# Performance work log

Hardware: AMD Instinct MI355X
Metric: run time of the kernel (lower is better)

The kernel has to match this reference:

```python
import jax, jax.numpy as jnp
import numpy as np

K = 3          # kernel size (implied by 18/27 offset channels)
PAD = 1
STRIDE = 1


def setup_inputs() -> dict:
    key = jax.random.key(0)
    k0, k1, k2 = jax.random.split(key, 3)
    B, C, H, W = 4, 256, 64, 64
    Cout = 256
    x = jax.random.normal(k0, (B, C, H, W), jnp.float32)
    # offset/mask predicting conv: 18 offset + 9 mask channels (deform_group=1)
    w_off = jax.random.normal(k1, (27, C, K, K), jnp.float32) * 0.01
    b_off = jnp.zeros((27,), jnp.float32)
    # main deformable conv weight (bias=False)
    w = jax.random.normal(k2, (Cout, C, K, K), jnp.float32) * 0.05
    return {"x": x, "w_off": w_off, "b_off": b_off, "w": w}


def _modulated_dcn(x, w_off, b_off, w):
    B, C, H, W = x.shape
    KK = K * K
    # regular conv predicting offsets (+ mask)
    om = jax.lax.conv_general_dilated(
        x, w_off, (STRIDE, STRIDE), [(PAD, PAD), (PAD, PAD)],
        dimension_numbers=("NCHW", "OIHW", "NCHW")) + b_off[None, :, None, None]
    Ho, Wo = om.shape[2], om.shape[3]
    # channel layout: interleaved (dy, dx) per kernel tap, then 9 mask channels
    off = om[:, :2 * KK].reshape(B, KK, 2, Ho, Wo)
    mask = jax.nn.sigmoid(om[:, 2 * KK:3 * KK])            # (B, KK, Ho, Wo)

    ky, kx = jnp.meshgrid(jnp.arange(K), jnp.arange(K), indexing="ij")
    base_y = (jnp.arange(Ho) * STRIDE - PAD)[:, None]       # (Ho, 1)
    base_x = (jnp.arange(Wo) * STRIDE - PAD)[None, :]       # (1, Wo)
    # sampling positions p = p0 + pn + offset, shape (B, KK, Ho, Wo)
    py = base_y[None, None] + ky.reshape(KK)[None, :, None, None] + off[:, :, 0]
    px = base_x[None, None] + kx.reshape(KK)[None, :, None, None] + off[:, :, 1]

    y0f = jnp.floor(py)
    x0f = jnp.floor(px)
    ly = py - y0f
    lx = px - x0f
    y0 = y0f.astype(jnp.int32)
    x0 = x0f.astype(jnp.int32)

    xf = x.reshape(B, C, H * W)

    def samp(yi, xi):
        valid = ((yi >= 0) & (yi < H) & (xi >= 0) & (xi < W)).astype(x.dtype)
        idx = jnp.clip(yi, 0, H - 1) * W + jnp.clip(xi, 0, W - 1)
        v = jnp.take_along_axis(xf, idx.reshape(B, 1, -1), axis=2)
        return v.reshape(B, C, KK, Ho, Wo) * valid[:, None]

    # bilinear interpolation with zero padding outside the image
    v = (samp(y0,     x0    ) * ((1 - ly) * (1 - lx))[:, None]
         + samp(y0,     x0 + 1) * ((1 - ly) * lx)[:, None]
         + samp(y0 + 1, x0    ) * (ly * (1 - lx))[:, None]
         + samp(y0 + 1, x0 + 1) * (ly * lx)[:, None])
    v = v * mask[:, None]                                   # modulation
    # conv as contraction over (Cin, KK)
    return jnp.einsum("bckhw,ock->bohw", v, w.reshape(w.shape[0], C, KK))


def reference(x, w_off, b_off, w):
    return _modulated_dcn(x, w_off, b_off, w)
```

## Files before the change

### kernel.cpp

```cpp
#include <hip/hip_runtime.h>
#include <math.h>

#define HH 64
#define WW 64
#define CIN 256
#define COUT 256
#define KKT 9
#define HWSZ 4096
#define VP 260

typedef __bf16  v8bf   __attribute__((ext_vector_type(8)));
typedef float   v4f    __attribute__((ext_vector_type(4)));
typedef short   short8 __attribute__((ext_vector_type(8)));
typedef unsigned short ushort4v __attribute__((ext_vector_type(4)));

__device__ inline unsigned short f2bf(float f) {
    union { float f; unsigned u; } uf; uf.f = f;
    unsigned r = uf.u + 0x7fff + ((uf.u >> 16) & 1);
    return (unsigned short)(r >> 16);
}
__device__ inline float bf2f(unsigned short u) {
    union { unsigned u; float f; } uf; uf.u = ((unsigned)u) << 16;
    return uf.f;
}

__global__ __launch_bounds__(256) void k_prep(const float* __restrict__ x,
                                              const float* __restrict__ w,
                                              const float* __restrict__ w_off,
                                              unsigned short* __restrict__ x_t,
                                              unsigned short* __restrict__ wprep,
                                              unsigned short* __restrict__ woffp) {
    __shared__ float s_w[2304];
    int id  = blockIdx.x;
    int tid = threadIdx.x;
    if (id < 256) {
        int b  = id >> 6;
        int h  = id & 63;
        int px  = tid & 63;
        int oct = tid >> 6;
        const float* xr = x + (((size_t)b * CIN) * HH + h) * WW;
        unsigned short* orow = x_t + (((size_t)id) * WW + px) * CIN;
        for (int g = 0; g < 8; g++) {
            int cb = g * 32 + oct * 8;
            unsigned short v[8];
#pragma unroll
            for (int j = 0; j < 8; j++)
                v[j] = f2bf(xr[(size_t)(cb + j) * HWSZ + px]);
            *(short8*)(orow + cb) = *(short8*)v;
        }
    } else if (id < 512) {
        int o = id - 256;
        for (int i = tid; i < 2304; i += 256) s_w[i] = w[(size_t)o * 2304 + i];
        __syncthreads();
        for (int u = tid; u < 576; u += 256) {
            int t  = u >> 3;
            int kq = u & 7;
            unsigned short v[4];
#pragma unroll
            for (int j = 0; j < 4; j++) {
                int kp = t * 32 + kq * 4 + j;
                int kk = kp >> 8;
                int c  = kp & 255;
                v[j] = f2bf(s_w[c * 9 + kk]);
            }
            *(ushort4v*)&wprep[((size_t)(t * 256 + o)) * 32 + kq * 4] = *(ushort4v*)v;
        }
    } else {
        int t = id - 512;
#pragma unroll
        for (int i = 0; i < 4; i++) {
            int idx = i * 256 + tid;
            int och = idx >> 5;
            int ki  = idx & 31;
            int kp  = t * 32 + ki;
            int kk  = kp >> 8;
            int c   = kp & 255;
            float v = (och < 27) ? w_off[((size_t)och * 256 + c) * 9 + kk] : 0.f;
            woffp[(size_t)t * 1024 + idx] = f2bf(v);
        }
    }
}

__global__ __launch_bounds__(512, 4) void k_main(const unsigned short* __restrict__ x_t,
                                                 const unsigned short* __restrict__ wprep,
                                                 const unsigned short* __restrict__ woffp,
                                                 const float* __restrict__ b_off,
                                                 float* __restrict__ out) {
    int id    = blockIdx.x;
    int g     = id & 7;
    int phalf = (id >> 3) & 1;
    int hi    = (id >> 4) & 7;
    int b     = id >> 7;
    int h     = g * 8 + hi;
    int p0    = phalf * 32;
    int tid  = threadIdx.x;
    int lane = tid & 63;
    int oct  = tid >> 6;
    int m16  = lane & 15;
    int quad = lane >> 4;

    __shared__ union {
        unsigned short v[2][32 * VP];
        float red[4][32][33];
    } s_u;
    __shared__ int4   s_base[KKT][32];
    __shared__ float4 s_wt  [KKT][32];

    const unsigned short* xb = x_t + (size_t)b * HWSZ * CIN;

    {
        int ks  = oct >> 1;
        int ntw = oct & 1;
        v4f aco[2];
        aco[0] = (v4f)(0.f);
        aco[1] = (v4f)(0.f);
#pragma unroll 3
        for (int j = 0; j < 18; j++) {
            int t  = j * 4 + ks;
            int kk = t >> 3;
            int ch = t & 7;
            int ky = kk / 3 - 1;
            int kx = kk - 3 * (kk / 3) - 1;
            const unsigned short* wp = woffp + (size_t)t * 1024;
            short8 af0 = *(const short8*)(wp + m16 * 32 + quad * 8);
            short8 af1 = *(const short8*)(wp + (16 + m16) * 32 + quad * 8);
            int y  = h + ky;
            int xg = p0 + ntw * 16 + m16 + kx;
            short8 bfr = (short8)0;
            if ((unsigned)y < HH && (unsigned)xg < WW)
                bfr = *(const short8*)(xb + ((size_t)y * WW + xg) * CIN + ch * 32 + quad * 8);
            aco[0] = __builtin_amdgcn_mfma_f32_16x16x32_bf16(
                __builtin_bit_cast(v8bf, af0), __builtin_bit_cast(v8bf, bfr), aco[0], 0, 0, 0);
            aco[1] = __builtin_amdgcn_mfma_f32_16x16x32_bf16(
                __builtin_bit_cast(v8bf, af1), __builtin_bit_cast(v8bf, bfr), aco[1], 0, 0, 0);
        }
#pragma unroll
        for (int mt = 0; mt < 2; mt++)
#pragma unroll
            for (int r = 0; r < 4; r++)
                s_u.red[ks][mt * 16 + quad * 4 + r][ntw * 16 + m16] = aco[mt][r];
    }
    __syncthreads();

    for (int i = tid; i < KKT * 32; i += 512) {
        int kk = i >> 5;
        int pl = i & 31;
        int p  = p0 + pl;
        float offy = s_u.red[0][2 * kk][pl]     + s_u.red[1][2 * kk][pl]
                   + s_u.red[2][2 * kk][pl]     + s_u.red[3][2 * kk][pl]     + b_off[2 * kk];
        float offx = s_u.red[0][2 * kk + 1][pl] + s_u.red[1][2 * kk + 1][pl]
                   + s_u.red[2][2 * kk + 1][pl] + s_u.red[3][2 * kk + 1][pl] + b_off[2 * kk + 1];
        float mv   = s_u.red[0][18 + kk][pl]    + s_u.red[1][18 + kk][pl]
                   + s_u.red[2][18 + kk][pl]    + s_u.red[3][18 + kk][pl]    + b_off[18 + kk];
        int ky = kk / 3, kx = kk - 3 * (kk / 3);
        float py = (float)(h - 1 + ky) + offy;
        float px = (float)(p - 1 + kx) + offx;
        float y0f = floorf(py);
        float x0f = floorf(px);
        float ly = py - y0f, lx = px - x0f;
        int y0 = (int)y0f, x0 = (int)x0f;
        float m = 1.f / (1.f + __expf(-mv));
        bool yv0 = (unsigned)y0       < HH;
        bool yv1 = (unsigned)(y0 + 1) < HH;
        bool xv0 = (unsigned)x0       < WW;
        bool xv1 = (unsigned)(x0 + 1) < WW;
        int y0c = min(max(y0, 0), HH - 1);
        int y1c = min(max(y0 + 1, 0), HH - 1);
        int x0c = min(max(x0, 0), WW - 1);
        int x1c = min(max(x0 + 1, 0), WW - 1);
        s_base[kk][pl] = make_int4((y0c * WW + x0c) * CIN, (y0c * WW + x1c) * CIN,
                                   (y1c * WW + x0c) * CIN, (y1c * WW + x1c) * CIN);
        s_wt[kk][pl] = make_float4(
            (yv0 && xv0) ? (1.f - ly) * (1.f - lx) * m : 0.f,
            (yv0 && xv1) ? (1.f - ly) * lx         * m : 0.f,
            (yv1 && xv0) ? ly * (1.f - lx)         * m : 0.f,
            (yv1 && xv1) ? ly * lx                 * m : 0.f);
    }
    __syncthreads();

    v4f acc[2][2];
#pragma unroll
    for (int mt = 0; mt < 2; mt++)
#pragma unroll
        for (int nt = 0; nt < 2; nt++) acc[mt][nt] = (v4f)(0.f);

    const unsigned short* xc = xb + lane * 4;

    for (int kk = 0; kk < KKT; kk++) {
        unsigned short* vbuf = s_u.v[kk & 1];

#pragma unroll
        for (int i = 0; i < 4; i++) {
            int pl = oct * 4 + i;
            int4   bp = s_base[kk][pl];
            float4 wt = s_wt[kk][pl];
            ushort4v t0 = *(const ushort4v*)(xc + bp.x);
            ushort4v t1 = *(const ushort4v*)(xc + bp.y);
            ushort4v t2 = *(const ushort4v*)(xc + bp.z);
            ushort4v t3 = *(const ushort4v*)(xc + bp.w);
            unsigned short vv[4];
#pragma unroll
            for (int j = 0; j < 4; j++) {
                float val = wt.x * bf2f(t0[j]) + wt.y * bf2f(t1[j])
                          + wt.z * bf2f(t2[j]) + wt.w * bf2f(t3[j]);
                vv[j] = f2bf(val);
            }
            *(ushort4v*)&vbuf[pl * VP + lane * 4] = *(ushort4v*)vv;
        }
        __syncthreads();

#pragma unroll
        for (int ch = 0; ch < 8; ch++) {
            int t = kk * 8 + ch;
            const unsigned short* wp = wprep + ((size_t)t * 256 + oct * 32) * 32;
            short8 af0 = *(const short8*)(wp + m16 * 32 + quad * 8);
            short8 af1 = *(const short8*)(wp + (16 + m16) * 32 + quad * 8);
            short8 bfr[2];
#pragma unroll
            for (int nt = 0; nt < 2; nt++)
                bfr[nt] = *(const short8*)&vbuf[(nt * 16 + m16) * VP + ch * 32 + quad * 8];
#pragma unroll
            for (int nt = 0; nt < 2; nt++) {
                acc[0][nt] = __builtin_amdgcn_mfma_f32_16x16x32_bf16(
                    __builtin_bit_cast(v8bf, af0), __builtin_bit_cast(v8bf, bfr[nt]),
                    acc[0][nt], 0, 0, 0);
                acc[1][nt] = __builtin_amdgcn_mfma_f32_16x16x32_bf16(
                    __builtin_bit_cast(v8bf, af1), __builtin_bit_cast(v8bf, bfr[nt]),
                    acc[1][nt], 0, 0, 0);
            }
        }
    }

    float* ob = out + ((size_t)b * COUT) * HWSZ + h * WW + p0;
#pragma unroll
    for (int mt = 0; mt < 2; mt++)
#pragma unroll
        for (int nt = 0; nt < 2; nt++)
#pragma unroll
            for (int r = 0; r < 4; r++) {
                int o = oct * 32 + mt * 16 + quad * 4 + r;
                ob[(size_t)o * HWSZ + nt * 16 + m16] = acc[mt][nt][r];
            }
}

extern "C" void kernel_launch(void* const* d_in, const int* in_sizes, int n_in,
                              void* d_out, int out_size, void* d_ws, size_t ws_size,
                              hipStream_t stream) {
    const float* x     = (const float*)d_in[0];
    const float* w_off = (const float*)d_in[1];
    const float* b_off = (const float*)d_in[2];
    const float* w     = (const float*)d_in[3];
    float* out = (float*)d_out;

    unsigned short* x_t   = (unsigned short*)d_ws;
    unsigned short* wprep = x_t + (size_t)4 * HWSZ * CIN;
    unsigned short* woffp = wprep + 589824;

    hipLaunchKernelGGL(k_prep, dim3(584), dim3(256), 0, stream, x, w, w_off, x_t, wprep, woffp);
    hipLaunchKernelGGL(k_main, dim3(512), dim3(512), 0, stream, x_t, wprep, woffp, b_off, out);
}
```

Measured before the change: 169.8 us.

## Fuse prep and main into one cooperative kernel with grid syncs and LDS staging

Merges the prep and main kernels into a single cooperative kernel that uses grid.sync() between phases. The x transpose now goes through an LDS tile so global reads are coalesced. The offset conv stages its 3-row input halo in LDS instead of issuing scattered global loads, and its result goes through a global om buffer. The aims are to remove a kernel launch, improve coalescing, and cut redundant global reads. In exchange it adds two grid-wide barriers, larger LDS use that may lower occupancy, single-buffered value staging with an extra barrier per tap, and a requirement that all 512 blocks be co-resident.

```diff
diff --git a/kernel.cpp b/kernel.cpp
--- a/kernel.cpp
+++ b/kernel.cpp
@@ -1,5 +1,8 @@
 #include <hip/hip_runtime.h>
+#include <hip/hip_cooperative_groups.h>
 #include <math.h>
+
+namespace cg = cooperative_groups;
 
 #define HH 64
 #define WW 64
@@ -8,11 +11,14 @@
 #define KKT 9
 #define HWSZ 4096
 #define VP 260
-
-typedef __bf16  v8bf   __attribute__((ext_vector_type(8)));
-typedef float   v4f    __attribute__((ext_vector_type(4)));
-typedef short   short8 __attribute__((ext_vector_type(8)));
+#define TP 258
+
+typedef __bf16  v8bf    __attribute__((ext_vector_type(8)));
+typedef float   v4f     __attribute__((ext_vector_type(4)));
+typedef short   short8  __attribute__((ext_vector_type(8)));
 typedef unsigned short ushort4v __attribute__((ext_vector_type(4)));
+typedef int     int4v   __attribute__((ext_vector_type(4)));
+typedef float   float4v __attribute__((ext_vector_type(4)));
 
 __device__ inline unsigned short f2bf(float f) {
     union { float f; unsigned u; } uf; uf.f = f;
@@ -24,35 +30,61 @@
     return uf.f;
 }
 
-__global__ __launch_bounds__(256) void k_prep(const float* __restrict__ x,
-                                              const float* __restrict__ w,
-                                              const float* __restrict__ w_off,
-                                              unsigned short* __restrict__ x_t,
-                                              unsigned short* __restrict__ wprep,
-                                              unsigned short* __restrict__ woffp) {
-    __shared__ float s_w[2304];
-    int id  = blockIdx.x;
-    int tid = threadIdx.x;
-    if (id < 256) {
-        int b  = id >> 6;
-        int h  = id & 63;
-        int px  = tid & 63;
-        int oct = tid >> 6;
-        const float* xr = x + (((size_t)b * CIN) * HH + h) * WW;
-        unsigned short* orow = x_t + (((size_t)id) * WW + px) * CIN;
-        for (int g = 0; g < 8; g++) {
-            int cb = g * 32 + oct * 8;
-            unsigned short v[8];
-#pragma unroll
-            for (int j = 0; j < 8; j++)
-                v[j] = f2bf(xr[(size_t)(cb + j) * HWSZ + px]);
-            *(short8*)(orow + cb) = *(short8*)v;
-        }
-    } else if (id < 512) {
-        int o = id - 256;
-        for (int i = tid; i < 2304; i += 256) s_w[i] = w[(size_t)o * 2304 + i];
-        __syncthreads();
-        for (int u = tid; u < 576; u += 256) {
+__global__ __launch_bounds__(512, 4) void k_fused(
+        const float* __restrict__ x, const float* __restrict__ w,
+        const float* __restrict__ w_off, const float* __restrict__ b_off,
+        unsigned short* __restrict__ x_t, unsigned short* __restrict__ wprep,
+        unsigned short* __restrict__ woffp, float* __restrict__ om,
+        float* __restrict__ out) {
+    cg::grid_group grid = cg::this_grid();
+
+    __shared__ union {
+        unsigned short t[64 * TP];
+        float w[2304];
+        struct { unsigned short row[3 * 34 * VP];
+                 float red[4][32][33]; } p2;
+        struct { int4v base[KKT][32]; float4v wt[KKT][32];
+                 unsigned short v[32 * VP]; } p3;
+    } s;
+
+    const int id    = blockIdx.x;
+    const int g     = id & 7;
+    const int phalf = (id >> 3) & 1;
+    const int hi    = (id >> 4) & 7;
+    const int b     = id >> 7;
+    const int h     = g * 8 + hi;
+    const int p0    = phalf * 32;
+    const int tid   = threadIdx.x;
+    const int lane  = tid & 63;
+    const int m16   = lane & 15;
+    const int quad  = lane >> 4;
+
+    if (phalf == 0) {
+#pragma unroll
+        for (int i = 0; i < 8; i++) {
+            int idx = i * 512 + tid;
+            int c   = idx >> 4;
+            int q   = idx & 15;
+            float4 v = *(const float4*)&x[(((size_t)b * CIN + c) * HH + h) * WW + q * 4];
+            s.t[(q * 4 + 0) * TP + c] = f2bf(v.x);
+            s.t[(q * 4 + 1) * TP + c] = f2bf(v.y);
+            s.t[(q * 4 + 2) * TP + c] = f2bf(v.z);
+            s.t[(q * 4 + 3) * TP + c] = f2bf(v.w);
+        }
+        __syncthreads();
+#pragma unroll
+        for (int i = 0; i < 4; i++) {
+            int idx = i * 512 + tid;
+            int px  = idx >> 5;
+            int c8  = idx & 31;
+            *(short8*)&x_t[(((size_t)(b * 64 + h)) * 64 + px) * CIN + c8 * 8] =
+                *(short8*)&s.t[px * TP + c8 * 8];
+        }
+    } else {
+        int o = (b << 6) | (hi << 3) | g;
+        for (int i = tid; i < 2304; i += 512) s.w[i] = w[(size_t)o * 2304 + i];
+        __syncthreads();
+        for (int u = tid; u < 576; u += 512) {
             int t  = u >> 3;
             int kq = u & 7;
             unsigned short v[4];
@@ -61,56 +93,46 @@
                 int kp = t * 32 + kq * 4 + j;
                 int kk = kp >> 8;
                 int c  = kp & 255;
-                v[j] = f2bf(s_w[c * 9 + kk]);
+                v[j] = f2bf(s.w[c * 9 + kk]);
             }
             *(ushort4v*)&wprep[((size_t)(t * 256 + o)) * 32 + kq * 4] = *(ushort4v*)v;
         }
-    } else {
-        int t = id - 512;
-#pragma unroll
-        for (int i = 0; i < 4; i++) {
-            int idx = i * 256 + tid;
-            int och = idx >> 5;
-            int ki  = idx & 31;
-            int kp  = t * 32 + ki;
-            int kk  = kp >> 8;
-            int c   = kp & 255;
-            float v = (och < 27) ? w_off[((size_t)och * 256 + c) * 9 + kk] : 0.f;
-            woffp[(size_t)t * 1024 + idx] = f2bf(v);
+        if (o < 72) {
+            int t = o;
+            for (int i = tid; i < 1024; i += 512) {
+                int och = i >> 5;
+                int ki  = i & 31;
+                int kp  = t * 32 + ki;
+                int kk  = kp >> 8;
+                int c   = kp & 255;
+                float v = (och < 27) ? w_off[((size_t)och * 256 + c) * 9 + kk] : 0.f;
+                woffp[(size_t)t * 1024 + i] = f2bf(v);
+            }
         }
     }
-}
-
-__global__ __launch_bounds__(512, 4) void k_main(const unsigned short* __restrict__ x_t,
-                                                 const unsigned short* __restrict__ wprep,
-                                                 const unsigned short* __restrict__ woffp,
-                                                 const float* __restrict__ b_off,
-                                                 float* __restrict__ out) {
-    int id    = blockIdx.x;
-    int g     = id & 7;
-    int phalf = (id >> 3) & 1;
-    int hi    = (id >> 4) & 7;
-    int b     = id >> 7;
-    int h     = g * 8 + hi;
-    int p0    = phalf * 32;
-    int tid  = threadIdx.x;
-    int lane = tid & 63;
-    int oct  = tid >> 6;
-    int m16  = lane & 15;
-    int quad = lane >> 4;
-
-    __shared__ union {
-        unsigned short v[2][32 * VP];
-        float red[4][32][33];
-    } s_u;
-    __shared__ int4   s_base[KKT][32];
-    __shared__ float4 s_wt  [KKT][32];
+    grid.sync();
 
     const unsigned short* xb = x_t + (size_t)b * HWSZ * CIN;
 
     {
-        int ks  = oct >> 1;
-        int ntw = oct & 1;
+        int wv  = tid >> 6;
+        int ks  = wv >> 1;
+        int ntw = wv & 1;
+
+        for (int u = tid; u < 3 * 1088; u += 512) {
+            int row = u / 1088;
+            int rem = u - row * 1088;
+            int px  = rem >> 5;
+            int c8  = (rem & 31) * 8;
+            int y   = h + row - 1;
+            int xg  = p0 + px - 1;
+            short8 val = (short8)0;
+            if ((unsigned)y < HH && (unsigned)xg < WW)
+                val = *(const short8*)(xb + ((size_t)y * WW + xg) * CIN + c8);
+            *(short8*)&s.p2.row[(row * 34 + px) * VP + c8] = val;
+        }
+        __syncthreads();
+
         v4f aco[2];
         aco[0] = (v4f)(0.f);
         aco[1] = (v4f)(0.f);
@@ -119,16 +141,13 @@
             int t  = j * 4 + ks;
             int kk = t >> 3;
             int ch = t & 7;
-            int ky = kk / 3 - 1;
-            int kx = kk - 3 * (kk / 3) - 1;
+            int ky = kk / 3;
+            int kx = kk - 3 * ky;
             const unsigned short* wp = woffp + (size_t)t * 1024;
             short8 af0 = *(const short8*)(wp + m16 * 32 + quad * 8);
             short8 af1 = *(const short8*)(wp + (16 + m16) * 32 + quad * 8);
-            int y  = h + ky;
-            int xg = p0 + ntw * 16 + m16 + kx;
-            short8 bfr = (short8)0;
-            if ((unsigned)y < HH && (unsigned)xg < WW)
-                bfr = *(const short8*)(xb + ((size_t)y * WW + xg) * CIN + ch * 32 + quad * 8);
+            short8 bfr = *(const short8*)
+                &s.p2.row[(ky * 34 + ntw * 16 + m16 + kx) * VP + ch * 32 + quad * 8];
             aco[0] = __builtin_amdgcn_mfma_f32_16x16x32_bf16(
                 __builtin_bit_cast(v8bf, af0), __builtin_bit_cast(v8bf, bfr), aco[0], 0, 0, 0);
             aco[1] = __builtin_amdgcn_mfma_f32_16x16x32_bf16(
@@ -138,109 +157,124 @@
         for (int mt = 0; mt < 2; mt++)
 #pragma unroll
             for (int r = 0; r < 4; r++)
-                s_u.red[ks][mt * 16 + quad * 4 + r][ntw * 16 + m16] = aco[mt][r];
+                s.p2.red[ks][mt * 16 + quad * 4 + r][ntw * 16 + m16] = aco[mt][r];
+        __syncthreads();
+
+        for (int i2 = tid; i2 < 27 * 32; i2 += 512) {
+            int och = i2 >> 5;
+            int px  = i2 & 31;
+            float sm = s.p2.red[0][och][px] + s.p2.red[1][och][px]
+                     + s.p2.red[2][och][px] + s.p2.red[3][och][px] + b_off[och];
+            om[((size_t)b * 27 + och) * HWSZ + h * WW + p0 + px] = sm;
+        }
     }
-    __syncthreads();
-
-    for (int i = tid; i < KKT * 32; i += 512) {
-        int kk = i >> 5;
-        int pl = i & 31;
-        int p  = p0 + pl;
-        float offy = s_u.red[0][2 * kk][pl]     + s_u.red[1][2 * kk][pl]
-                   + s_u.red[2][2 * kk][pl]     + s_u.red[3][2 * kk][pl]     + b_off[2 * kk];
-        float offx = s_u.red[0][2 * kk + 1][pl] + s_u.red[1][2 * kk + 1][pl]
-                   + s_u.red[2][2 * kk + 1][pl] + s_u.red[3][2 * kk + 1][pl] + b_off[2 * kk + 1];
-        float mv   = s_u.red[0][18 + kk][pl]    + s_u.red[1][18 + kk][pl]
-                   + s_u.red[2][18 + kk][pl]    + s_u.red[3][18 + kk][pl]    + b_off[18 + kk];
-        int ky = kk / 3, kx = kk - 3 * (kk / 3);
-        float py = (float)(h - 1 + ky) + offy;
-        float px = (float)(p - 1 + kx) + offx;
-        float y0f = floorf(py);
-        float x0f = floorf(px);
-        float ly = py - y0f, lx = px - x0f;
-        int y0 = (int)y0f, x0 = (int)x0f;
-        float m = 1.f / (1.f + __expf(-mv));
-        bool yv0 = (unsigned)y0       < HH;
-        bool yv1 = (unsigned)(y0 + 1) < HH;
-        bool xv0 = (unsigned)x0       < WW;
-        bool xv1 = (unsigned)(x0 + 1) < WW;
-        int y0c = min(max(y0, 0), HH - 1);
-        int y1c = min(max(y0 + 1, 0), HH - 1);
-        int x0c = min(max(x0, 0), WW - 1);
-        int x1c = min(max(x0 + 1, 0), WW - 1);
-        s_base[kk][pl] = make_int4((y0c * WW + x0c) * CIN, (y0c * WW + x1c) * CIN,
-                                   (y1c * WW + x0c) * CIN, (y1c * WW + x1c) * CIN);
-        s_wt[kk][pl] = make_float4(
-            (yv0 && xv0) ? (1.f - ly) * (1.f - lx) * m : 0.f,
-            (yv0 && xv1) ? (1.f - ly) * lx         * m : 0.f,
-            (yv1 && xv0) ? ly * (1.f - lx)         * m : 0.f,
-            (yv1 && xv1) ? ly * lx                 * m : 0.f);
+    grid.sync();
+
+    {
+        int oct = tid >> 6;
+
+        const float* omb = om + (size_t)b * 27 * HWSZ + h * WW;
+        for (int i = tid; i < KKT * 32; i += 512) {
+            int kk = i >> 5;
+            int pl = i & 31;
+            int p  = p0 + pl;
+            float offy = omb[(size_t)(2 * kk)     * HWSZ + p];
+            float offx = omb[(size_t)(2 * kk + 1) * HWSZ + p];
+            float mv   = omb[(size_t)(18 + kk)    * HWSZ + p];
+            int ky = kk / 3, kx = kk - 3 * (kk / 3);
+            float py = (float)(h - 1 + ky) + offy;
+            float px = (float)(p - 1 + kx) + offx;
+            float y0f = floorf(py);
+            float x0f = floorf(px);
+            float ly = py - y0f, lx = px - x0f;
+            int y0 = (int)y0f, x0 = (int)x0f;
+            float m = 1.f / (1.f + __expf(-mv));
+            bool yv0 = (unsigned)y0       < HH;
+            bool yv1 = (unsigned)(y0 + 1) < HH;
+            bool xv0 = (unsigned)x0       < WW;
+            bool xv1 = (unsigned)(x0 + 1) < WW;
+            int y0c = min(max(y0, 0), HH - 1);
+            int y1c = min(max(y0 + 1, 0), HH - 1);
+            int x0c = min(max(x0, 0), WW - 1);
+            int x1c = min(max(x0 + 1, 0), WW - 1);
+            int4v bse;
+            bse.x = (y0c * WW + x0c) * CIN;
+            bse.y = (y0c * WW + x1c) * CIN;
+            bse.z = (y1c * WW + x0c) * CIN;
+            bse.w = (y1c * WW + x1c) * CIN;
+            s.p3.base[kk][pl] = bse;
+            float4v wt;
+            wt.x = (yv0 && xv0) ? (1.f - ly) * (1.f - lx) * m : 0.f;
+            wt.y = (yv0 && xv1) ? (1.f - ly) * lx         * m : 0.f;
+            wt.z = (yv1 && xv0) ? ly * (1.f - lx)         * m : 0.f;
+            wt.w = (yv1 && xv1) ? ly * lx                 * m : 0.f;
+            s.p3.wt[kk][pl] = wt;
+        }
+        __syncthreads();
+
+        v4f acc[2][2];
+#pragma unroll
+        for (int mt = 0; mt < 2; mt++)
+#pragma unroll
+            for (int nt = 0; nt < 2; nt++) acc[mt][nt] = (v4f)(0.f);
+
+        const unsigned short* xc = xb + lane * 4;
+
+        for (int kk = 0; kk < KKT; kk++) {
+#pragma unroll
+            for (int i = 0; i < 4; i++) {
+                int pl = oct * 4 + i;
+                int4v   bp = s.p3.base[kk][pl];
+                float4v wt = s.p3.wt[kk][pl];
+                ushort4v t0 = *(const ushort4v*)(xc + bp.x);
+                ushort4v t1 = *(const ushort4v*)(xc + bp.y);
+                ushort4v t2 = *(const ushort4v*)(xc + bp.z);
+                ushort4v t3 = *(const ushort4v*)(xc + bp.w);
+                unsigned short vv[4];
+#pragma unroll
+                for (int j = 0; j < 4; j++) {
+                    float val = wt.x * bf2f(t0[j]) + wt.y * bf2f(t1[j])
+                              + wt.z * bf2f(t2[j]) + wt.w * bf2f(t3[j]);
+                    vv[j] = f2bf(val);
+                }
+                *(ushort4v*)&s.p3.v[pl * VP + lane * 4] = *(ushort4v*)vv;
+            }
+            __syncthreads();
+
+#pragma unroll 2
+            for (int ch = 0; ch < 8; ch++) {
+                int t = kk * 8 + ch;
+                const unsigned short* wp = wprep + ((size_t)t * 256 + oct * 32) * 32;
+                short8 af0 = *(const short8*)(wp + m16 * 32 + quad * 8);
+                short8 af1 = *(const short8*)(wp + (16 + m16) * 32 + quad * 8);
+                short8 bfr[2];
+#pragma unroll
+                for (int nt = 0; nt < 2; nt++)
+                    bfr[nt] = *(const short8*)&s.p3.v[(nt * 16 + m16) * VP + ch * 32 + quad * 8];
+#pragma unroll
+                for (int nt = 0; nt < 2; nt++) {
+                    acc[0][nt] = __builtin_amdgcn_mfma_f32_16x16x32_bf16(
+                        __builtin_bit_cast(v8bf, af0), __builtin_bit_cast(v8bf, bfr[nt]),
+                        acc[0][nt], 0, 0, 0);
+                    acc[1][nt] = __builtin_amdgcn_mfma_f32_16x16x32_bf16(
+                        __builtin_bit_cast(v8bf, af1), __builtin_bit_cast(v8bf, bfr[nt]),
+                        acc[1][nt], 0, 0, 0);
+                }
+            }
+            __syncthreads();
+        }
+
+        float* ob = out + ((size_t)b * COUT) * HWSZ + h * WW + p0;
+#pragma unroll
+        for (int mt = 0; mt < 2; mt++)
+#pragma unroll
+            for (int nt = 0; nt < 2; nt++)
+#pragma unroll
+                for (int r = 0; r < 4; r++) {
+                    int o = oct * 32 + mt * 16 + quad * 4 + r;
+                    ob[(size_t)o * HWSZ + nt * 16 + m16] = acc[mt][nt][r];
+                }
     }
-    __syncthreads();
-
-    v4f acc[2][2];
-#pragma unroll
-    for (int mt = 0; mt < 2; mt++)
-#pragma unroll
-        for (int nt = 0; nt < 2; nt++) acc[mt][nt] = (v4f)(0.f);
-
-    const unsigned short* xc = xb + lane * 4;
-
-    for (int kk = 0; kk < KKT; kk++) {
-        unsigned short* vbuf = s_u.v[kk & 1];
-
-#pragma unroll
-        for (int i = 0; i < 4; i++) {
-            int pl = oct * 4 + i;
-            int4   bp = s_base[kk][pl];
-            float4 wt = s_wt[kk][pl];
-            ushort4v t0 = *(const ushort4v*)(xc + bp.x);
-            ushort4v t1 = *(const ushort4v*)(xc + bp.y);
-            ushort4v t2 = *(const ushort4v*)(xc + bp.z);
-            ushort4v t3 = *(const ushort4v*)(xc + bp.w);
-            unsigned short vv[4];
-#pragma unroll
-            for (int j = 0; j < 4; j++) {
-                float val = wt.x * bf2f(t0[j]) + wt.y * bf2f(t1[j])
-                          + wt.z * bf2f(t2[j]) + wt.w * bf2f(t3[j]);
-                vv[j] = f2bf(val);
-            }
-            *(ushort4v*)&vbuf[pl * VP + lane * 4] = *(ushort4v*)vv;
-        }
-        __syncthreads();
-
-#pragma unroll
-        for (int ch = 0; ch < 8; ch++) {
-            int t = kk * 8 + ch;
-            const unsigned short* wp = wprep + ((size_t)t * 256 + oct * 32) * 32;
-            short8 af0 = *(const short8*)(wp + m16 * 32 + quad * 8);
-            short8 af1 = *(const short8*)(wp + (16 + m16) * 32 + quad * 8);
-            short8 bfr[2];
-#pragma unroll
-            for (int nt = 0; nt < 2; nt++)
-                bfr[nt] = *(const short8*)&vbuf[(nt * 16 + m16) * VP + ch * 32 + quad * 8];
-#pragma unroll
-            for (int nt = 0; nt < 2; nt++) {
-                acc[0][nt] = __builtin_amdgcn_mfma_f32_16x16x32_bf16(
-                    __builtin_bit_cast(v8bf, af0), __builtin_bit_cast(v8bf, bfr[nt]),
-                    acc[0][nt], 0, 0, 0);
-                acc[1][nt] = __builtin_amdgcn_mfma_f32_16x16x32_bf16(
-                    __builtin_bit_cast(v8bf, af1), __builtin_bit_cast(v8bf, bfr[nt]),
-                    acc[1][nt], 0, 0, 0);
-            }
-        }
-    }
-
-    float* ob = out + ((size_t)b * COUT) * HWSZ + h * WW + p0;
-#pragma unroll
-    for (int mt = 0; mt < 2; mt++)
-#pragma unroll
-        for (int nt = 0; nt < 2; nt++)
-#pragma unroll
-            for (int r = 0; r < 4; r++) {
-                int o = oct * 32 + mt * 16 + quad * 4 + r;
-                ob[(size_t)o * HWSZ + nt * 16 + m16] = acc[mt][nt][r];
-            }
 }
 
 extern "C" void kernel_launch(void* const* d_in, const int* in_sizes, int n_in,
@@ -252,10 +286,13 @@
     const float* w     = (const float*)d_in[3];
     float* out = (float*)d_out;
 
-    unsigned short* x_t   = (unsigned short*)d_ws;
+    float* om = (float*)d_ws;
+    unsigned short* x_t   = (unsigned short*)(om + 442368);
     unsigned short* wprep = x_t + (size_t)4 * HWSZ * CIN;
     unsigned short* woffp = wprep + 589824;
 
-    hipLaunchKernelGGL(k_prep, dim3(584), dim3(256), 0, stream, x, w, w_off, x_t, wprep, woffp);
-    hipLaunchKernelGGL(k_main, dim3(512), dim3(512), 0, stream, x_t, wprep, woffp, b_off, out);
-}
+    void* args[] = {(void*)&x, (void*)&w, (void*)&w_off, (void*)&b_off,
+                    (void*)&x_t, (void*)&wprep, (void*)&woffp, (void*)&om,
+                    (void*)&out};
+    hipLaunchCooperativeKernel((void*)k_fused, dim3(512), dim3(512), args, 0, stream);
+}
```

Result: slower. 286.0 us (+68.4%).
